# Optimization experiments

Measured on AMD Instinct MI355X. Metric: run time of the kernel, lower is better.

Reference implementation:

```python
import jax, jax.numpy as jnp
import numpy as np

B = 16384
F_IN = 768
F_OUT = 512

def setup_inputs() -> dict:
    key = jax.random.key(0)
    k1, k2, k3, k4, k5, k6 = jax.random.split(key, 6)
    # densified sparse multi-hot boards (post to_dense())
    stm = jax.random.uniform(k1, (B, F_IN), dtype=jnp.float32)
    nstm = jax.random.uniform(k2, (B, F_IN), dtype=jnp.float32)
    s1 = 1.0 / np.sqrt(F_IN)
    s2 = 1.0 / np.sqrt(2 * F_OUT)
    W1 = jax.random.normal(k3, (F_OUT, F_IN), dtype=jnp.float32) * s1
    b1 = jax.random.normal(k4, (F_OUT,), dtype=jnp.float32) * s1
    W2 = jax.random.normal(k5, (1, 2 * F_OUT), dtype=jnp.float32) * s2
    b2 = jax.random.normal(k6, (1,), dtype=jnp.float32) * s2
    return {"stm": stm, "nstm": nstm, "W1": W1, "b1": b1, "W2": W2, "b2": b2}

def reference(stm, nstm, W1, b1, W2, b2):
    # shared feature transformer applied to both perspectives
    stm_p = stm @ W1.T + b1    # [B, F_OUT]
    nstm_p = nstm @ W1.T + b1  # [B, F_OUT]
    hidden = jnp.clip(jnp.concatenate((stm_p, nstm_p), axis=1), 0.0, 1.0)  # [B, 2*F_OUT]
    return jax.nn.sigmoid(hidden @ W2.T + b2)  # [B, 1]
```

## Files before the change

### kernel.cpp

```cpp
#include <hip/hip_runtime.h>
#include <hip/hip_bf16.h>

#define BATCH 16384
#define FIN   768
#define FOUT  512

#define BM 128
#define BN 256
#define BK 32
#define LDK 40
#define W1B_OFF 65536

typedef __attribute__((ext_vector_type(8))) short short8;
typedef __attribute__((ext_vector_type(4))) float floatx4;

__device__ __forceinline__ unsigned int cvt_pk_bf16(float a, float b) {
    unsigned int r;
    asm("v_cvt_pk_bf16_f32 %0, %1, %2" : "=v"(r) : "v"(a), "v"(b));
    return r;
}

__device__ __forceinline__ uint2 pack4(float4 v) {
    uint2 o;
    o.x = cvt_pk_bf16(v.x, v.y);
    o.y = cvt_pk_bf16(v.z, v.w);
    return o;
}

__global__ __launch_bounds__(256) void cvt_w1(
    const float* __restrict__ W1, unsigned short* __restrict__ W1b)
{
    int base = (blockIdx.x * 256 + threadIdx.x) * 8;
    float4 a = *(const float4*)(W1 + base);
    float4 b = *(const float4*)(W1 + base + 4);
    uint4 o;
    uint2 pa = pack4(a), pb = pack4(b);
    o.x = pa.x; o.y = pa.y; o.z = pb.x; o.w = pb.y;
    *(uint4*)(W1b + base) = o;
}

__global__ __launch_bounds__(512, 4) void pn_gemm(
    const float* __restrict__ stm, const float* __restrict__ nstm,
    const unsigned short* __restrict__ W1b, const float* __restrict__ b1,
    const float* __restrict__ W2, float* __restrict__ ws)
{
    __shared__ __align__(16) unsigned short As[BM * LDK];
    __shared__ __align__(16) unsigned short Bs[BN * LDK];

    const int tid  = threadIdx.x;
    const int lane = tid & 63;
    const int wave = tid >> 6;
    const int wm   = wave >> 2;
    const int wn   = wave & 3;
    const int quad = lane >> 4;
    const int l16  = lane & 15;

    const int id = blockIdx.x;
    const int w4 = id & 15;
    const int rowTileIdx = (id >> 4) * 8 + (w4 & 7);
    const int colTile    = (w4 >> 3) * BN;
    const int rowTile    = rowTileIdx * BM;

    const int p = (rowTile >= BATCH) ? 1 : 0;
    const float* __restrict__ X = p ? nstm : stm;
    const int rowOff = rowTile - p * BATCH;

    const int arow = tid >> 3;
    const int asp4 = tid & 7;
    const int bcol = tid >> 2;
    const int bc16 = tid & 3;

    const float* aPtr = X + (size_t)(rowOff + arow) * FIN + asp4 * 4;
    const unsigned short* bPtr = W1b + (size_t)(colTile + bcol) * FIN + bc16 * 8;

    floatx4 acc[4][4];
    #pragma unroll
    for (int i = 0; i < 4; ++i)
        #pragma unroll
        for (int j = 0; j < 4; ++j)
            acc[i][j] = (floatx4)0.0f;

    for (int kt = 0; kt < FIN; kt += BK) {
        __syncthreads();
        #pragma unroll
        for (int i = 0; i < 2; ++i) {
            float4 v = *(const float4*)(aPtr + kt + (size_t)(i * 64) * FIN);
            *(uint2*)(&As[(arow + i * 64) * LDK + asp4 * 4]) = pack4(v);
        }
        #pragma unroll
        for (int i = 0; i < 2; ++i) {
            uint4 v = *(const uint4*)(bPtr + kt + (size_t)(i * 128) * FIN);
            *(uint4*)(&Bs[(bcol + i * 128) * LDK + bc16 * 8]) = v;
        }
        __syncthreads();

        short8 af[4], bfr[4];
        #pragma unroll
        for (int mi = 0; mi < 4; ++mi)
            af[mi] = *(const short8*)(&As[(wm * 64 + mi * 16 + l16) * LDK + quad * 8]);
        #pragma unroll
        for (int ni = 0; ni < 4; ++ni)
            bfr[ni] = *(const short8*)(&Bs[(wn * 64 + ni * 16 + l16) * LDK + quad * 8]);

        #pragma unroll
        for (int mi = 0; mi < 4; ++mi)
            #pragma unroll
            for (int ni = 0; ni < 4; ++ni)
                acc[mi][ni] = __builtin_amdgcn_mfma_f32_16x16x32_bf16(
                    af[mi], bfr[ni], acc[mi][ni], 0, 0, 0);
    }

    float b1v[4], w2v[4];
    #pragma unroll
    for (int ni = 0; ni < 4; ++ni) {
        int col = colTile + wn * 64 + ni * 16 + l16;
        b1v[ni] = b1[col];
        w2v[ni] = W2[p * FOUT + col];
    }

    const int rBase = rowOff + wm * 64;
    #pragma unroll
    for (int mi = 0; mi < 4; ++mi) {
        #pragma unroll
        for (int r = 0; r < 4; ++r) {
            float s = 0.0f;
            #pragma unroll
            for (int ni = 0; ni < 4; ++ni) {
                float h = acc[mi][ni][r] + b1v[ni];
                h = fminf(fmaxf(h, 0.0f), 1.0f);
                s += h * w2v[ni];
            }
            s += __shfl_xor(s, 1);
            s += __shfl_xor(s, 2);
            s += __shfl_xor(s, 4);
            s += __shfl_xor(s, 8);
            if (l16 == 0) {
                atomicAdd(&ws[rBase + mi * 16 + quad * 4 + r], s);
            }
        }
    }
}

__global__ __launch_bounds__(256) void pn_finalize(
    const float* __restrict__ ws, const float* __restrict__ b2,
    float* __restrict__ out)
{
    int i = blockIdx.x * blockDim.x + threadIdx.x;
    float x = ws[i] + b2[0];
    out[i] = 1.0f / (1.0f + expf(-x));
}

extern "C" void kernel_launch(void* const* d_in, const int* in_sizes, int n_in,
                              void* d_out, int out_size, void* d_ws, size_t ws_size,
                              hipStream_t stream)
{
    (void)in_sizes; (void)n_in; (void)out_size; (void)ws_size;
    const float* stm  = (const float*)d_in[0];
    const float* nstm = (const float*)d_in[1];
    const float* W1   = (const float*)d_in[2];
    const float* b1   = (const float*)d_in[3];
    const float* W2   = (const float*)d_in[4];
    const float* b2   = (const float*)d_in[5];
    float* out = (float*)d_out;
    float* ws  = (float*)d_ws;
    unsigned short* W1b = (unsigned short*)((char*)d_ws + W1B_OFF);

    hipMemsetAsync(ws, 0, BATCH * sizeof(float), stream);
    cvt_w1<<<dim3((FOUT * FIN) / (256 * 8)), dim3(256), 0, stream>>>(W1, W1b);

    dim3 grid((FOUT / BN) * ((2 * BATCH) / BM));
    pn_gemm<<<grid, dim3(512), 0, stream>>>(stm, nstm, W1b, b1, W2, ws);
    pn_finalize<<<dim3(BATCH / 256), dim3(256), 0, stream>>>(ws, b2, out);
}
```

Before: 162.5 us.

## Load W1 tiles via global_load_lds with XOR swizzle, retile to 128x128x64

The bf16 W1 tile now goes straight from global memory into LDS through global_load_lds, bypassing registers, and uses an XOR-swizzled layout so the fragment reads avoid bank conflicts without padding. The block tile changes from 128x256x32 with 512 threads to 128x128x64 with 256 threads, giving two MFMA k-substeps per barrier pair and doubling the grid. This halves the number of K iterations and synchronisations, but the activation matrix is now re-read by twice as many column tiles, which raises global A traffic.

After: 161.6 us. No clear change (-0.5%).

```diff
diff --git a/kernel.cpp b/kernel.cpp
--- a/kernel.cpp
+++ b/kernel.cpp
@@ -6,9 +6,10 @@
 #define FOUT  512
 
 #define BM 128
-#define BN 256
-#define BK 32
-#define LDK 40
+#define BN 128
+#define BK 64
+#define LDKA 72
+#define NT (FIN / BK)
 #define W1B_OFF 65536
 
 typedef __attribute__((ext_vector_type(8))) short short8;
@@ -27,51 +28,57 @@
     return o;
 }
 
+__device__ __forceinline__ void load_lds_16(const void* g, void* l) {
+    __builtin_amdgcn_global_load_lds(
+        (const __attribute__((address_space(1))) unsigned int*)g,
+        (__attribute__((address_space(3))) unsigned int*)l,
+        16, 0, 0);
+}
+
 __global__ __launch_bounds__(256) void cvt_w1(
     const float* __restrict__ W1, unsigned short* __restrict__ W1b)
 {
     int base = (blockIdx.x * 256 + threadIdx.x) * 8;
     float4 a = *(const float4*)(W1 + base);
     float4 b = *(const float4*)(W1 + base + 4);
-    uint4 o;
     uint2 pa = pack4(a), pb = pack4(b);
-    o.x = pa.x; o.y = pa.y; o.z = pb.x; o.w = pb.y;
+    uint4 o; o.x = pa.x; o.y = pa.y; o.z = pb.x; o.w = pb.y;
     *(uint4*)(W1b + base) = o;
 }
 
-__global__ __launch_bounds__(512, 4) void pn_gemm(
+__global__ __launch_bounds__(256, 4) void pn_gemm(
     const float* __restrict__ stm, const float* __restrict__ nstm,
     const unsigned short* __restrict__ W1b, const float* __restrict__ b1,
     const float* __restrict__ W2, float* __restrict__ ws)
 {
-    __shared__ __align__(16) unsigned short As[BM * LDK];
-    __shared__ __align__(16) unsigned short Bs[BN * LDK];
+    __shared__ __align__(16) unsigned short As[BM * LDKA];
+    __shared__ __align__(16) unsigned short Bs[BN * BK];
 
     const int tid  = threadIdx.x;
     const int lane = tid & 63;
     const int wave = tid >> 6;
-    const int wm   = wave >> 2;
-    const int wn   = wave & 3;
+    const int wm   = wave >> 1;
+    const int wn   = wave & 1;
     const int quad = lane >> 4;
     const int l16  = lane & 15;
 
     const int id = blockIdx.x;
-    const int w4 = id & 15;
-    const int rowTileIdx = (id >> 4) * 8 + (w4 & 7);
-    const int colTile    = (w4 >> 3) * BN;
+    const int g  = id >> 5;
+    const int w5 = id & 31;
+    const int rowTileIdx = g * 8 + (w5 & 7);
+    const int colTile    = (w5 >> 3) * BN;
     const int rowTile    = rowTileIdx * BM;
 
     const int p = (rowTile >= BATCH) ? 1 : 0;
     const float* __restrict__ X = p ? nstm : stm;
     const int rowOff = rowTile - p * BATCH;
 
-    const int arow = tid >> 3;
-    const int asp4 = tid & 7;
-    const int bcol = tid >> 2;
-    const int bc16 = tid & 3;
+    const int arow = tid >> 4;
+    const int asp4 = tid & 15;
+    const float* aPtr = X + (size_t)(rowOff + arow) * FIN + asp4 * 4;
 
-    const float* aPtr = X + (size_t)(rowOff + arow) * FIN + asp4 * 4;
-    const unsigned short* bPtr = W1b + (size_t)(colTile + bcol) * FIN + bc16 * 8;
+    const int bRowInJ = lane >> 3;
+    const int bgc     = (lane & 7) ^ bRowInJ;
 
     floatx4 acc[4][4];
     #pragma unroll
@@ -80,34 +87,44 @@
         for (int j = 0; j < 4; ++j)
             acc[i][j] = (floatx4)0.0f;
 
-    for (int kt = 0; kt < FIN; kt += BK) {
+    for (int t = 0; t < NT; ++t) {
+        const int kt = t * BK;
         __syncthreads();
+
         #pragma unroll
-        for (int i = 0; i < 2; ++i) {
-            float4 v = *(const float4*)(aPtr + kt + (size_t)(i * 64) * FIN);
-            *(uint2*)(&As[(arow + i * 64) * LDK + asp4 * 4]) = pack4(v);
+        for (int i = 0; i < 4; ++i) {
+            const int J = wave + i * 4;
+            const int row = J * 8 + bRowInJ;
+            load_lds_16(W1b + (size_t)(colTile + row) * FIN + kt + bgc * 8,
+                        &Bs[J * 512]);
         }
         #pragma unroll
-        for (int i = 0; i < 2; ++i) {
-            uint4 v = *(const uint4*)(bPtr + kt + (size_t)(i * 128) * FIN);
-            *(uint4*)(&Bs[(bcol + i * 128) * LDK + bc16 * 8]) = v;
+        for (int i = 0; i < 8; ++i) {
+            float4 v = *(const float4*)(aPtr + kt + (size_t)(i * 16) * FIN);
+            *(uint2*)(&As[(arow + i * 16) * LDKA + asp4 * 4]) = pack4(v);
         }
         __syncthreads();
 
-        short8 af[4], bfr[4];
         #pragma unroll
-        for (int mi = 0; mi < 4; ++mi)
-            af[mi] = *(const short8*)(&As[(wm * 64 + mi * 16 + l16) * LDK + quad * 8]);
-        #pragma unroll
-        for (int ni = 0; ni < 4; ++ni)
-            bfr[ni] = *(const short8*)(&Bs[(wn * 64 + ni * 16 + l16) * LDK + quad * 8]);
-
-        #pragma unroll
-        for (int mi = 0; mi < 4; ++mi)
+        for (int s = 0; s < 2; ++s) {
+            short8 af[4], bfr[4];
             #pragma unroll
-            for (int ni = 0; ni < 4; ++ni)
-                acc[mi][ni] = __builtin_amdgcn_mfma_f32_16x16x32_bf16(
-                    af[mi], bfr[ni], acc[mi][ni], 0, 0, 0);
+            for (int mi = 0; mi < 4; ++mi)
+                af[mi] = *(const short8*)(
+                    &As[(wm * 64 + mi * 16 + l16) * LDKA + s * 32 + quad * 8]);
+            #pragma unroll
+            for (int ni = 0; ni < 4; ++ni) {
+                const int r = wn * 64 + ni * 16 + l16;
+                bfr[ni] = *(const short8*)(
+                    &Bs[r * 64 + (((s * 4 + quad) ^ (r & 7)) * 8)]);
+            }
+            #pragma unroll
+            for (int mi = 0; mi < 4; ++mi)
+                #pragma unroll
+                for (int ni = 0; ni < 4; ++ni)
+                    acc[mi][ni] = __builtin_amdgcn_mfma_f32_16x16x32_bf16(
+                        af[mi], bfr[ni], acc[mi][ni], 0, 0, 0);
+        }
     }
 
     float b1v[4], w2v[4];
@@ -169,6 +186,6 @@
     cvt_w1<<<dim3((FOUT * FIN) / (256 * 8)), dim3(256), 0, stream>>>(W1, W1b);
 
     dim3 grid((FOUT / BN) * ((2 * BATCH) / BM));
-    pn_gemm<<<grid, dim3(512), 0, stream>>>(stm, nstm, W1b, b1, W2, ws);
+    pn_gemm<<<grid, dim3(256), 0, stream>>>(stm, nstm, W1b, b1, W2, ws);
     pn_finalize<<<dim3(BATCH / 256), dim3(256), 0, stream>>>(ws, b2, out);
 }
```
